# Kernel tuning notes

Measured on AMD Instinct MI355X. Metric: run time of the kernel, lower is better.

The kernel has to match this reference:

```python
import jax, jax.numpy as jnp
import numpy as np

EPS_BN = 1e-5
EPS_SIM = 1e-8
PAD = 1
NUM_ITERS = 3


def capsule_conv2d(x, w):
    # x: [B, C, H, W]; w: [out_caps, in_caps, kh, kw, in_len, out_len]
    B, C, H, W = x.shape
    oc, ic, kh, kw, il, ol = w.shape
    # im2col patches, feature dim ordered (c, kh, kw) -> matches torch.unfold
    patches = jax.lax.conv_general_dilated_patches(
        x, (kh, kw), (1, 1), [(PAD, PAD), (PAD, PAD)])  # [B, C*kh*kw, H, W]
    N = H * W
    p = patches.reshape(B, ic, il, kh * kw, N)
    p = jnp.transpose(p, (0, 4, 1, 3, 2))  # [B, N, ic, kk, il]
    wf = w.reshape(oc, ic, kh * kw, il, ol)
    # per-patch capsule transform -> priors [B, N, oc, ic*kk, ol]
    priors = jnp.einsum('bnikl,oiklm->bnoikm', p, wf)
    priors = priors.reshape(B, N, oc, ic * kh * kw, ol)
    # k-means routing with Tonimoto similarity, 3 iterations, no squash
    out = priors.mean(axis=-2, keepdims=True)  # [B, N, oc, 1, ol]
    for _ in range(NUM_ITERS):
        dot = jnp.sum(priors * out, axis=-1, keepdims=True)
        n1 = jnp.sum(priors * priors, axis=-1, keepdims=True)
        n2 = jnp.sum(out * out, axis=-1, keepdims=True)
        logits = dot / jnp.maximum(n1 + n2 - dot, EPS_SIM)
        probs = jax.nn.softmax(logits, axis=-2)
        out = jnp.sum(probs * priors, axis=-2, keepdims=True)
    out = out[..., 0, :]                      # [B, N, oc, ol]
    out = out.reshape(B, H, W, oc * ol)       # channels = oc*ol
    return jnp.transpose(out, (0, 3, 1, 2))   # [B, C, H, W]


def batchnorm2d(x, gamma, beta):
    mean = x.mean(axis=(0, 2, 3), keepdims=True)
    var = x.var(axis=(0, 2, 3), keepdims=True)  # biased, as torch BN training fwd
    inv = jax.lax.rsqrt(var + EPS_BN)
    return gamma[None, :, None, None] * (x - mean) * inv + beta[None, :, None, None]


def setup_inputs() -> dict:
    key = jax.random.key(0)
    k0, k1, k2 = jax.random.split(key, 3)
    B, C, H, W = 2, 64, 96, 96
    IL = OL = 8
    x = jax.random.normal(k0, (B, C, H, W), jnp.float32)
    w1 = jax.random.normal(k1, (C // OL, C // IL, 3, 3, IL, OL), jnp.float32) * 0.1
    w2 = jax.random.normal(k2, (C // OL, C // OL, 3, 3, OL, OL), jnp.float32) * 0.1
    g1 = jnp.ones((C,), jnp.float32)
    b1 = jnp.zeros((C,), jnp.float32)
    g2 = jnp.ones((C,), jnp.float32)
    b2 = jnp.zeros((C,), jnp.float32)
    return {"x": x, "w1": w1, "g1": g1, "b1": b1, "w2": w2, "g2": g2, "b2": b2}


def reference(x, w1, g1, b1, w2, g2, b2):
    r = batchnorm2d(capsule_conv2d(x, w1), g1, b1)
    r = batchnorm2d(capsule_conv2d(r, w2), g2, b2)
    return x + r
```

## Files before the change

### kernel.cpp

```cpp
#include <hip/hip_runtime.h>
#include <hip/hip_bf16.h>

#define HW 9216
#define NPC 18432
#define NELEM 1179648
#define PSTR 584
#define XSTR 72
#define PATCH_B 7776
#define PRL_O 18688

typedef __attribute__((ext_vector_type(2))) float f32x2;
typedef __attribute__((ext_vector_type(4))) float f32x4v;
typedef __attribute__((ext_vector_type(8))) short short8v;

__device__ __forceinline__ f32x2 fma2(f32x2 a, f32x2 b, f32x2 c) {
#if __has_builtin(__builtin_elementwise_fma)
    return __builtin_elementwise_fma(a, b, c);
#else
    return f32x2{fmaf(a.x, b.x, c.x), fmaf(a.y, b.y, c.y)};
#endif
}
__device__ __forceinline__ float dot8v(f32x2 a0, f32x2 a1, f32x2 a2, f32x2 a3,
                                       f32x2 b0, f32x2 b1, f32x2 b2, f32x2 b3) {
    f32x2 acc = a0 * b0;
    acc = fma2(a1, b1, acc);
    acc = fma2(a2, b2, acc);
    acc = fma2(a3, b3, acc);
    return acc.x + acc.y;
}

template <int CTRL>
__device__ __forceinline__ float dpp_add(float x) {
    int y = __builtin_amdgcn_update_dpp(0, __float_as_int(x), CTRL, 0xF, 0xF, true);
    return x + __int_as_float(y);
}
template <int CTRL>
__device__ __forceinline__ f32x2 dpp_add2(f32x2 x) {
    int ya = __builtin_amdgcn_update_dpp(0, __float_as_int(x.x), CTRL, 0xF, 0xF, true);
    int yb = __builtin_amdgcn_update_dpp(0, __float_as_int(x.y), CTRL, 0xF, 0xF, true);
    return x + f32x2{__int_as_float(ya), __int_as_float(yb)};
}
__device__ __forceinline__ float red_lo(float x) {
    x = dpp_add<0xB1>(x);
    x = dpp_add<0x4E>(x);
    x = dpp_add<0x141>(x);
    return x;
}
__device__ __forceinline__ f32x2 red_lo2(f32x2 x) {
    x = dpp_add2<0xB1>(x);
    x = dpp_add2<0x4E>(x);
    x = dpp_add2<0x141>(x);
    return x;
}

__device__ __forceinline__ int detect_is32(const unsigned short* __restrict__ w1u) {
    int lane = threadIdx.x & 63;
    int bad = 0;
    #pragma unroll
    for (int i = 0; i < 16; ++i) {
        unsigned short u = (unsigned short)(w1u[lane + i * 64] & 0x7FFF);
        bad |= (u >= 0x42C8);
    }
    return (__ballot(bad) != 0ULL) ? 1 : 0;
}

__device__ __forceinline__ float load_in(const void* p, int idx, int is32) {
    return is32 ? ((const float*)p)[idx]
                : __bfloat162float(((const __hip_bfloat16*)p)[idx]);
}

__device__ __forceinline__ float lo16(unsigned v) { return __int_as_float((int)(v << 16)); }
__device__ __forceinline__ float hi16(unsigned v) { return __int_as_float((int)(v & 0xFFFF0000u)); }
__device__ __forceinline__ unsigned pk2bf(float a, float b) {
    __hip_bfloat162 h = __float22bfloat162_rn(float2{a, b});
    return *(unsigned*)&h;
}

__launch_bounds__(256)
__global__ void prep_kernel(const void* __restrict__ x,
                            const void* __restrict__ w1, const void* __restrict__ w2,
                            __hip_bfloat16* __restrict__ xt,
                            __hip_bfloat16* __restrict__ Bfr1,
                            __hip_bfloat16* __restrict__ Bfr2,
                            float* __restrict__ statz) {
    __shared__ float tile[64 * 33];
    const int bid = blockIdx.x;
    if (bid < 576) {
        const int is32 = detect_is32((const unsigned short*)w1);
        int xb = bid % 3, y = (bid / 3) % 96, b = bid / 288;
        int x0 = xb * 32;
        for (int e = threadIdx.x; e < 2048; e += 256) {
            int xl = e & 31, c = e >> 5;
            tile[c * 33 + xl] = load_in(x, ((b * 64 + c) * 96 + y) * 96 + x0 + xl, is32);
        }
        __syncthreads();
        for (int f = threadIdx.x; f < 1024; f += 256) {
            int c2 = f & 31, xl = f >> 5;
            float a = tile[(2 * c2) * 33 + xl];
            float c = tile[(2 * c2 + 1) * 33 + xl];
            *(unsigned*)&xt[((b * 96 + y) * 96 + x0 + xl) * 64 + 2 * c2] = pk2bf(a, c);
        }
    } else if (bid < 720) {
        const int is32 = detect_is32((const unsigned short*)w1);
        int t = (bid - 576) * 256 + threadIdx.x;
        int layer = t / 18432;
        int r = t - layer * 18432;
        int lane = r & 63;
        int fi = r >> 6;
        int h = fi & 1, g = (fi >> 1) & 1;
        int kq = fi >> 2;
        int k = kq % 9, o = kq / 9;
        int dy = k / 3, dx = k % 3;
        int quad = lane >> 4, colhi = (lane >> 3) & 1, m = lane & 7;
        int act = (quad == 2 * h + colhi);
        int i = g * 4 + 2 * h + colhi;
        const void* w = layer ? w2 : w1;
        __hip_bfloat16* dst = layer ? Bfr2 : Bfr1;
        #pragma unroll
        for (int j = 0; j < 8; ++j) {
            float v = act ? load_in(w, ((((o * 8 + i) * 3 + dy) * 3 + dx) * 8 + j) * 8 + m, is32)
                          : 0.f;
            dst[(fi * 64 + lane) * 8 + j] = __float2bfloat16(v);
        }
    } else {
        for (int e = threadIdx.x; e < 2048; e += 256) statz[e] = 0.f;
    }
}

__launch_bounds__(256, 3)
__global__ void caps_kernel(const __hip_bfloat16* __restrict__ in,
                            const float* __restrict__ statPrev,
                            const void* __restrict__ gamma, const void* __restrict__ beta,
                            const void* __restrict__ wdt,
                            const __hip_bfloat16* __restrict__ Bfr,
                            __hip_bfloat16* __restrict__ yout,
                            float* __restrict__ statL,
                            int layer1) {
    __shared__ __align__(16) unsigned char smem[PATCH_B + 2 * PRL_O];
    __hip_bfloat16* patchH = (__hip_bfloat16*)smem;
    __hip_bfloat16* prH    = (__hip_bfloat16*)(smem + PATCH_B);
    float* omF = (float*)smem;
    float* scL = (float*)(smem + PATCH_B);
    float* shL = scL + 64;

    const int gx    = blockIdx.x;
    const int opair = gx & 3;
    const int x0    = (gx >> 2) * 16;
    const int y  = blockIdx.y;
    const int b  = blockIdx.z;
    const int tid = threadIdx.x;

    if (!layer1) {
        if (tid < 64) {
            const int is32 = detect_is32((const unsigned short*)wdt);
            int c = tid;
            float s = 0.f, ss = 0.f;
            #pragma unroll
            for (int cp = 0; cp < 8; ++cp) {
                s  += statPrev[cp * 128 + c];
                ss += statPrev[cp * 128 + 64 + c];
            }
            float mean = s * (1.f / (float)NPC);
            float var  = fmaxf(ss * (1.f / (float)NPC) - mean * mean, 0.f);
            float inv  = rsqrtf(var + 1e-5f);
            float g = load_in(gamma, c, is32) * inv;
            scL[c] = g;
            shL[c] = load_in(beta, c, is32) - mean * g;
        }
        __syncthreads();
    }

    for (int e = tid; e < 864; e += 256) {
        int c4 = e & 15;
        int q  = e >> 4;
        int xo = q % 18, row = q / 18;
        int yy = y + row - 1, xx = x0 + xo - 1;
        uint2 v = {0u, 0u};
        if (yy >= 0 && yy < 96 && xx >= 0 && xx < 96) {
            v = *(const uint2*)&in[((b * 96 + yy) * 96 + xx) * 64 + c4 * 4];
            if (!layer1) {
                int c = c4 * 4;
                float f0 = lo16(v.x) * scL[c]     + shL[c];
                float f1 = hi16(v.x) * scL[c + 1] + shL[c + 1];
                float f2 = lo16(v.y) * scL[c + 2] + shL[c + 2];
                float f3 = hi16(v.y) * scL[c + 3] + shL[c + 3];
                v.x = pk2bf(f0, f1);
                v.y = pk2bf(f2, f3);
            }
        }
        *(uint2*)&patchH[q * XSTR + c4 * 4] = v;
    }
    __syncthreads();

    const int lane = tid & 63;
    const int wv   = tid >> 6;
    const int o2w  = wv >> 1;
    const int g    = wv & 1;

    {
        const int o     = opair * 2 + o2w;
        const int pos16 = lane & 15;
        const int quad  = lane >> 4;
        const int mbase = (quad & 1) * 4;
        const int ihl   = quad >> 1;
        __hip_bfloat16* prBase = prH + o2w * 9344;
        #pragma unroll
        for (int k = 0; k < 9; ++k) {
            const int dy = k / 3, dx = k % 3;
            short8v a = *(const short8v*)&patchH[(dy * 18 + dx + pos16) * XSTR + g * 32 + quad * 8];
            #pragma unroll
            for (int h = 0; h < 2; ++h) {
                short8v bf = *(const short8v*)&Bfr[((((o * 9 + k) * 2 + g) * 2 + h) * 64 + lane) * 8];
                f32x4v d = __builtin_amdgcn_mfma_f32_16x16x32_bf16(bf, a, (f32x4v){0.f, 0.f, 0.f, 0.f}, 0, 0, 0);
                const int iw = g * 4 + 2 * h + ihl;
                uint2 pk;
                pk.x = pk2bf(d[0], d[1]);
                pk.y = pk2bf(d[2], d[3]);
                *(uint2*)&prBase[pos16 * PSTR + (iw * 9 + k) * 8 + mbase] = pk;
            }
        }
    }
    __syncthreads();

    const int unit = tid >> 3;
    const int o2   = unit >> 4;
    const int pos  = unit & 15;
    const int i    = tid & 7;
    const __hip_bfloat16* pb = &prH[o2 * 9344 + pos * PSTR + i * 72];

    uint4 u[9];
    #pragma unroll
    for (int k = 0; k < 9; ++k) u[k] = *(const uint4*)(pb + k * 8);

    f32x2 fr[36];
    float n1[9];
    #pragma unroll
    for (int k = 0; k < 9; ++k) {
        fr[4 * k + 0] = f32x2{lo16(u[k].x), hi16(u[k].x)};
        fr[4 * k + 1] = f32x2{lo16(u[k].y), hi16(u[k].y)};
        fr[4 * k + 2] = f32x2{lo16(u[k].z), hi16(u[k].z)};
        fr[4 * k + 3] = f32x2{lo16(u[k].w), hi16(u[k].w)};
    }

    f32x2 om2[4];
    {
        f32x2 s2[4] = {f32x2{0.f, 0.f}, f32x2{0.f, 0.f}, f32x2{0.f, 0.f}, f32x2{0.f, 0.f}};
        #pragma unroll
        for (int k = 0; k < 9; ++k) {
            s2[0] += fr[4 * k + 0];
            s2[1] += fr[4 * k + 1];
            s2[2] += fr[4 * k + 2];
            s2[3] += fr[4 * k + 3];
        }
        #pragma unroll
        for (int q = 0; q < 4; ++q) {
            f32x2 t = red_lo2(s2[q]);
            om2[q] = t * f32x2{1.f / 72.f, 1.f / 72.f};
        }
    }
    float n2 = dot8v(om2[0], om2[1], om2[2], om2[3], om2[0], om2[1], om2[2], om2[3]);

    #pragma unroll
    for (int it = 0; it < 3; ++it) {
        float se = 0.f;
        f32x2 acc2[4] = {f32x2{0.f, 0.f}, f32x2{0.f, 0.f}, f32x2{0.f, 0.f}, f32x2{0.f, 0.f}};
        #pragma unroll
        for (int k = 0; k < 9; ++k) {
            if (it == 0)
                n1[k] = dot8v(fr[4 * k], fr[4 * k + 1], fr[4 * k + 2], fr[4 * k + 3],
                              fr[4 * k], fr[4 * k + 1], fr[4 * k + 2], fr[4 * k + 3]);
            float d = dot8v(fr[4 * k], fr[4 * k + 1], fr[4 * k + 2], fr[4 * k + 3],
                            om2[0], om2[1], om2[2], om2[3]);
            float denom = fmaxf(n1[k] + n2 - d, 1e-8f);
            float e = __expf(d * __builtin_amdgcn_rcpf(denom));
            se += e;
            f32x2 ev{e, e};
            acc2[0] = fma2(ev, fr[4 * k + 0], acc2[0]);
            acc2[1] = fma2(ev, fr[4 * k + 1], acc2[1]);
            acc2[2] = fma2(ev, fr[4 * k + 2], acc2[2]);
            acc2[3] = fma2(ev, fr[4 * k + 3], acc2[3]);
        }
        se = red_lo(se);
        #pragma unroll
        for (int q = 0; q < 4; ++q) acc2[q] = red_lo2(acc2[q]);
        float inv = __builtin_amdgcn_rcpf(se);
        f32x2 iv{inv, inv};
        #pragma unroll
        for (int q = 0; q < 4; ++q) om2[q] = acc2[q] * iv;
        n2 = dot8v(om2[0], om2[1], om2[2], om2[3], om2[0], om2[1], om2[2], om2[3]);
    }

    if (i == 0) {
        const int o = opair * 2 + o2;
        uint4 pk;
        pk.x = pk2bf(om2[0].x, om2[0].y);
        pk.y = pk2bf(om2[1].x, om2[1].y);
        pk.z = pk2bf(om2[2].x, om2[2].y);
        pk.w = pk2bf(om2[3].x, om2[3].y);
        *(uint4*)&yout[((b * 96 + y) * 96 + x0 + pos) * 64 + o * 8] = pk;
        float4 o0 = {om2[0].x, om2[0].y, om2[1].x, om2[1].y};
        float4 o1 = {om2[2].x, om2[2].y, om2[3].x, om2[3].y};
        *(float4*)&omF[unit * 8] = o0;
        *(float4*)&omF[unit * 8 + 4] = o1;
    }
    __syncthreads();

    if (tid < 32) {
        int c16 = tid & 15, sel = tid >> 4;
        int oo2 = c16 >> 3, m = c16 & 7;
        float v = 0.f;
        #pragma unroll
        for (int pp = 0; pp < 16; ++pp) {
            float t = omF[(oo2 * 16 + pp) * 8 + m];
            v += sel ? t * t : t;
        }
        int cp = (blockIdx.x + blockIdx.y * 3 + blockIdx.z) & 7;
        atomicAdd(&statL[cp * 128 + sel * 64 + (opair * 2 + oo2) * 8 + m], v);
    }
}

__launch_bounds__(256)
__global__ void final_kernel(const void* __restrict__ xin,
                             const __hip_bfloat16* __restrict__ yt2,
                             const float* __restrict__ statL,
                             const void* __restrict__ gamma, const void* __restrict__ beta,
                             const void* __restrict__ w1,
                             void* __restrict__ outp) {
    __shared__ float tile[64 * 33];
    __shared__ float scL[64], shL[64];
    const int is32 = detect_is32((const unsigned short*)w1);
    if (threadIdx.x < 64) {
        int c = threadIdx.x;
        float s = 0.f, ss = 0.f;
        #pragma unroll
        for (int cp = 0; cp < 8; ++cp) {
            s  += statL[cp * 128 + c];
            ss += statL[cp * 128 + 64 + c];
        }
        float mean = s * (1.f / (float)NPC);
        float var  = fmaxf(ss * (1.f / (float)NPC) - mean * mean, 0.f);
        float inv  = rsqrtf(var + 1e-5f);
        float g = load_in(gamma, c, is32) * inv;
        scL[c] = g;
        shL[c] = load_in(beta, c, is32) - mean * g;
    }
    __syncthreads();

    int x0 = blockIdx.x * 32, y = blockIdx.y, b = blockIdx.z;
    for (int e = threadIdx.x; e < 1024; e += 256) {
        int c2 = e & 31, xl = e >> 5;
        unsigned v = *(const unsigned*)&yt2[((b * 96 + y) * 96 + x0 + xl) * 64 + c2 * 2];
        int c = c2 * 2;
        tile[c * 33 + xl]       = lo16(v) * scL[c]     + shL[c];
        tile[(c + 1) * 33 + xl] = hi16(v) * scL[c + 1] + shL[c + 1];
    }
    __syncthreads();
    for (int f = threadIdx.x; f < 2048; f += 256) {
        int xl = f & 31, c = f >> 5;
        int idx = ((b * 64 + c) * 96 + y) * 96 + x0 + xl;
        float v = load_in(xin, idx, is32) + tile[c * 33 + xl];
        if (is32) ((float*)outp)[idx] = v;
        else      ((__hip_bfloat16*)outp)[idx] = __float2bfloat16(v);
    }
}

extern "C" void kernel_launch(void* const* d_in, const int* in_sizes, int n_in,
                              void* d_out, int out_size, void* d_ws, size_t ws_size,
                              hipStream_t stream) {
    const void* x  = d_in[0];
    const void* w1 = d_in[1];
    const void* g1 = d_in[2];
    const void* b1 = d_in[3];
    const void* w2 = d_in[4];
    const void* g2 = d_in[5];
    const void* b2 = d_in[6];

    __hip_bfloat16* bufA = (__hip_bfloat16*)d_ws;
    __hip_bfloat16* bufB = bufA + NELEM;
    __hip_bfloat16* Bfr1 = bufB + NELEM;
    __hip_bfloat16* Bfr2 = Bfr1 + 147456;
    float* statz = (float*)(Bfr2 + 147456);
    float* statL1 = statz;
    float* statL2 = statz + 1024;

    prep_kernel<<<721, 256, 0, stream>>>(x, w1, w2, bufA, Bfr1, Bfr2, statz);

    dim3 cgrid(24, 96, 2);
    caps_kernel<<<cgrid, 256, 0, stream>>>(bufA, nullptr, nullptr, nullptr, w1,
                                           Bfr1, bufB, statL1, 1);
    caps_kernel<<<cgrid, 256, 0, stream>>>(bufB, statL1, g1, b1, w1,
                                           Bfr2, bufA, statL2, 0);
    final_kernel<<<dim3(3, 96, 2), 256, 0, stream>>>(x, bufA, statL2, g2, b2, w1, d_out);
}
```

Before: 175.7 us.

## Split capsule routing to one output capsule per block, two threads per row

Each caps_kernel block now handles a single output capsule instead of a pair, so the grid doubles and shared memory for priors halves. Within routing, each (position, input-capsule) pair is split across two threads that each take about half of the 9 kernel taps, with an extra DPP reduction step across 16 lanes. The aim is to cut per-thread register pressure (fr drops from 36 to 20 vectors) and raise occupancy (launch bounds 3→4 blocks). The cost is that patch loading and BN-apply work is repeated twice as often across blocks, plus a padded fifth tap slot and an extra reduction stage.

Result: slower. 187.1 us (+6.5%).

```diff
diff --git a/kernel.cpp b/kernel.cpp
--- a/kernel.cpp
+++ b/kernel.cpp
@@ -40,16 +40,18 @@
     int yb = __builtin_amdgcn_update_dpp(0, __float_as_int(x.y), CTRL, 0xF, 0xF, true);
     return x + f32x2{__int_as_float(ya), __int_as_float(yb)};
 }
-__device__ __forceinline__ float red_lo(float x) {
+__device__ __forceinline__ float red16(float x) {
     x = dpp_add<0xB1>(x);
     x = dpp_add<0x4E>(x);
     x = dpp_add<0x141>(x);
+    x = dpp_add<0x140>(x);
     return x;
 }
-__device__ __forceinline__ f32x2 red_lo2(f32x2 x) {
+__device__ __forceinline__ f32x2 red16_2(f32x2 x) {
     x = dpp_add2<0xB1>(x);
     x = dpp_add2<0x4E>(x);
     x = dpp_add2<0x141>(x);
+    x = dpp_add2<0x140>(x);
     return x;
 }
 
@@ -127,7 +129,7 @@
     }
 }
 
-__launch_bounds__(256, 3)
+__launch_bounds__(256, 4)
 __global__ void caps_kernel(const __hip_bfloat16* __restrict__ in,
                             const float* __restrict__ statPrev,
                             const void* __restrict__ gamma, const void* __restrict__ beta,
@@ -136,16 +138,16 @@
                             __hip_bfloat16* __restrict__ yout,
                             float* __restrict__ statL,
                             int layer1) {
-    __shared__ __align__(16) unsigned char smem[PATCH_B + 2 * PRL_O];
+    __shared__ __align__(16) unsigned char smem[PATCH_B + PRL_O];
     __hip_bfloat16* patchH = (__hip_bfloat16*)smem;
     __hip_bfloat16* prH    = (__hip_bfloat16*)(smem + PATCH_B);
     float* omF = (float*)smem;
     float* scL = (float*)(smem + PATCH_B);
     float* shL = scL + 64;
 
-    const int gx    = blockIdx.x;
-    const int opair = gx & 3;
-    const int x0    = (gx >> 2) * 16;
+    const int gx = blockIdx.x;
+    const int o  = gx & 7;
+    const int x0 = (gx >> 3) * 16;
     const int y  = blockIdx.y;
     const int b  = blockIdx.z;
     const int tid = threadIdx.x;
@@ -194,95 +196,91 @@
 
     const int lane = tid & 63;
     const int wv   = tid >> 6;
-    const int o2w  = wv >> 1;
-    const int g    = wv & 1;
 
     {
-        const int o     = opair * 2 + o2w;
+        const int g = wv & 1;
+        const int h = wv >> 1;
         const int pos16 = lane & 15;
         const int quad  = lane >> 4;
         const int mbase = (quad & 1) * 4;
         const int ihl   = quad >> 1;
-        __hip_bfloat16* prBase = prH + o2w * 9344;
+        const int iw    = g * 4 + 2 * h + ihl;
         #pragma unroll
         for (int k = 0; k < 9; ++k) {
             const int dy = k / 3, dx = k % 3;
             short8v a = *(const short8v*)&patchH[(dy * 18 + dx + pos16) * XSTR + g * 32 + quad * 8];
-            #pragma unroll
-            for (int h = 0; h < 2; ++h) {
-                short8v bf = *(const short8v*)&Bfr[((((o * 9 + k) * 2 + g) * 2 + h) * 64 + lane) * 8];
-                f32x4v d = __builtin_amdgcn_mfma_f32_16x16x32_bf16(bf, a, (f32x4v){0.f, 0.f, 0.f, 0.f}, 0, 0, 0);
-                const int iw = g * 4 + 2 * h + ihl;
-                uint2 pk;
-                pk.x = pk2bf(d[0], d[1]);
-                pk.y = pk2bf(d[2], d[3]);
-                *(uint2*)&prBase[pos16 * PSTR + (iw * 9 + k) * 8 + mbase] = pk;
-            }
-        }
-    }
-    __syncthreads();
-
-    const int unit = tid >> 3;
-    const int o2   = unit >> 4;
-    const int pos  = unit & 15;
-    const int i    = tid & 7;
-    const __hip_bfloat16* pb = &prH[o2 * 9344 + pos * PSTR + i * 72];
-
-    uint4 u[9];
+            short8v bf = *(const short8v*)&Bfr[((((o * 9 + k) * 2 + g) * 2 + h) * 64 + lane) * 8];
+            f32x4v d = __builtin_amdgcn_mfma_f32_16x16x32_bf16(bf, a, (f32x4v){0.f, 0.f, 0.f, 0.f}, 0, 0, 0);
+            uint2 pk;
+            pk.x = pk2bf(d[0], d[1]);
+            pk.y = pk2bf(d[2], d[3]);
+            *(uint2*)&prH[pos16 * PSTR + (iw * 9 + k) * 8 + mbase] = pk;
+        }
+    }
+    __syncthreads();
+
+    const int pos = tid >> 4;
+    const int i   = tid & 7;
+    const int kh  = (tid >> 3) & 1;
+    const __hip_bfloat16* pb = &prH[pos * PSTR + i * 72];
+
+    uint4 u[5];
     #pragma unroll
-    for (int k = 0; k < 9; ++k) u[k] = *(const uint4*)(pb + k * 8);
-
-    f32x2 fr[36];
-    float n1[9];
+    for (int t = 0; t < 4; ++t) u[t] = *(const uint4*)(pb + (kh + 2 * t) * 8);
+    u[4] = *(const uint4*)(pb + 8 * 8);
+    if (kh) { u[4].x = 0u; u[4].y = 0u; u[4].z = 0u; u[4].w = 0u; }
+
+    f32x2 fr[20];
+    float n1[5];
     #pragma unroll
-    for (int k = 0; k < 9; ++k) {
-        fr[4 * k + 0] = f32x2{lo16(u[k].x), hi16(u[k].x)};
-        fr[4 * k + 1] = f32x2{lo16(u[k].y), hi16(u[k].y)};
-        fr[4 * k + 2] = f32x2{lo16(u[k].z), hi16(u[k].z)};
-        fr[4 * k + 3] = f32x2{lo16(u[k].w), hi16(u[k].w)};
+    for (int t = 0; t < 5; ++t) {
+        fr[4 * t + 0] = f32x2{lo16(u[t].x), hi16(u[t].x)};
+        fr[4 * t + 1] = f32x2{lo16(u[t].y), hi16(u[t].y)};
+        fr[4 * t + 2] = f32x2{lo16(u[t].z), hi16(u[t].z)};
+        fr[4 * t + 3] = f32x2{lo16(u[t].w), hi16(u[t].w)};
     }
 
     f32x2 om2[4];
     {
         f32x2 s2[4] = {f32x2{0.f, 0.f}, f32x2{0.f, 0.f}, f32x2{0.f, 0.f}, f32x2{0.f, 0.f}};
         #pragma unroll
-        for (int k = 0; k < 9; ++k) {
-            s2[0] += fr[4 * k + 0];
-            s2[1] += fr[4 * k + 1];
-            s2[2] += fr[4 * k + 2];
-            s2[3] += fr[4 * k + 3];
+        for (int t = 0; t < 5; ++t) {
+            s2[0] += fr[4 * t + 0];
+            s2[1] += fr[4 * t + 1];
+            s2[2] += fr[4 * t + 2];
+            s2[3] += fr[4 * t + 3];
         }
         #pragma unroll
         for (int q = 0; q < 4; ++q) {
-            f32x2 t = red_lo2(s2[q]);
-            om2[q] = t * f32x2{1.f / 72.f, 1.f / 72.f};
+            f32x2 tt = red16_2(s2[q]);
+            om2[q] = tt * f32x2{1.f / 72.f, 1.f / 72.f};
         }
     }
     float n2 = dot8v(om2[0], om2[1], om2[2], om2[3], om2[0], om2[1], om2[2], om2[3]);
 
     #pragma unroll
     for (int it = 0; it < 3; ++it) {
-        float se = 0.f;
+        float se = kh ? -1.f : 0.f;
         f32x2 acc2[4] = {f32x2{0.f, 0.f}, f32x2{0.f, 0.f}, f32x2{0.f, 0.f}, f32x2{0.f, 0.f}};
         #pragma unroll
-        for (int k = 0; k < 9; ++k) {
+        for (int t = 0; t < 5; ++t) {
             if (it == 0)
-                n1[k] = dot8v(fr[4 * k], fr[4 * k + 1], fr[4 * k + 2], fr[4 * k + 3],
-                              fr[4 * k], fr[4 * k + 1], fr[4 * k + 2], fr[4 * k + 3]);
-            float d = dot8v(fr[4 * k], fr[4 * k + 1], fr[4 * k + 2], fr[4 * k + 3],
+                n1[t] = dot8v(fr[4 * t], fr[4 * t + 1], fr[4 * t + 2], fr[4 * t + 3],
+                              fr[4 * t], fr[4 * t + 1], fr[4 * t + 2], fr[4 * t + 3]);
+            float d = dot8v(fr[4 * t], fr[4 * t + 1], fr[4 * t + 2], fr[4 * t + 3],
                             om2[0], om2[1], om2[2], om2[3]);
-            float denom = fmaxf(n1[k] + n2 - d, 1e-8f);
+            float denom = fmaxf(n1[t] + n2 - d, 1e-8f);
             float e = __expf(d * __builtin_amdgcn_rcpf(denom));
             se += e;
             f32x2 ev{e, e};
-            acc2[0] = fma2(ev, fr[4 * k + 0], acc2[0]);
-            acc2[1] = fma2(ev, fr[4 * k + 1], acc2[1]);
-            acc2[2] = fma2(ev, fr[4 * k + 2], acc2[2]);
-            acc2[3] = fma2(ev, fr[4 * k + 3], acc2[3]);
-        }
-        se = red_lo(se);
-        #pragma unroll
-        for (int q = 0; q < 4; ++q) acc2[q] = red_lo2(acc2[q]);
+            acc2[0] = fma2(ev, fr[4 * t + 0], acc2[0]);
+            acc2[1] = fma2(ev, fr[4 * t + 1], acc2[1]);
+            acc2[2] = fma2(ev, fr[4 * t + 2], acc2[2]);
+            acc2[3] = fma2(ev, fr[4 * t + 3], acc2[3]);
+        }
+        se = red16(se);
+        #pragma unroll
+        for (int q = 0; q < 4; ++q) acc2[q] = red16_2(acc2[q]);
         float inv = __builtin_amdgcn_rcpf(se);
         f32x2 iv{inv, inv};
         #pragma unroll
@@ -290,8 +288,7 @@
         n2 = dot8v(om2[0], om2[1], om2[2], om2[3], om2[0], om2[1], om2[2], om2[3]);
     }
 
-    if (i == 0) {
-        const int o = opair * 2 + o2;
+    if ((tid & 15) == 0) {
         uint4 pk;
         pk.x = pk2bf(om2[0].x, om2[0].y);
         pk.y = pk2bf(om2[1].x, om2[1].y);
@@ -300,22 +297,21 @@
         *(uint4*)&yout[((b * 96 + y) * 96 + x0 + pos) * 64 + o * 8] = pk;
         float4 o0 = {om2[0].x, om2[0].y, om2[1].x, om2[1].y};
         float4 o1 = {om2[2].x, om2[2].y, om2[3].x, om2[3].y};
-        *(float4*)&omF[unit * 8] = o0;
-        *(float4*)&omF[unit * 8 + 4] = o1;
-    }
-    __syncthreads();
-
-    if (tid < 32) {
-        int c16 = tid & 15, sel = tid >> 4;
-        int oo2 = c16 >> 3, m = c16 & 7;
+        *(float4*)&omF[pos * 8] = o0;
+        *(float4*)&omF[pos * 8 + 4] = o1;
+    }
+    __syncthreads();
+
+    if (tid < 16) {
+        int m = tid & 7, sel = tid >> 3;
         float v = 0.f;
         #pragma unroll
         for (int pp = 0; pp < 16; ++pp) {
-            float t = omF[(oo2 * 16 + pp) * 8 + m];
+            float t = omF[pp * 8 + m];
             v += sel ? t * t : t;
         }
         int cp = (blockIdx.x + blockIdx.y * 3 + blockIdx.z) & 7;
-        atomicAdd(&statL[cp * 128 + sel * 64 + (opair * 2 + oo2) * 8 + m], v);
+        atomicAdd(&statL[cp * 128 + sel * 64 + o * 8 + m], v);
     }
 }
 
@@ -385,7 +381,7 @@
 
     prep_kernel<<<721, 256, 0, stream>>>(x, w1, w2, bufA, Bfr1, Bfr2, statz);
 
-    dim3 cgrid(24, 96, 2);
+    dim3 cgrid(48, 96, 2);
     caps_kernel<<<cgrid, 256, 0, stream>>>(bufA, nullptr, nullptr, nullptr, w1,
                                            Bfr1, bufB, statL1, 1);
     caps_kernel<<<cgrid, 256, 0, stream>>>(bufB, statL1, g1, b1, w1,
```

## Keep capsule priors in MFMA registers and route with cross-lane shuffles

Applied to the files above, without the earlier changes.

The capsule transform's MFMA outputs now stay in registers in their native MFMA layout. The bf16 round-trip through a large LDS prior buffer is gone. The routing iterations do their dot products and weighted sums with lane shuffles, plus a small LDS exchange between the two waves that hold different input-capsule halves, with a block barrier per iteration. LDS use shrinks, so occupancy rises to 4 blocks per CU. The price is extra syncthreads and shuffles per iteration, and each wave does redundant routing math.

After: 165.5 us. -5.8%, faster.

```diff
diff --git a/kernel.cpp b/kernel.cpp
--- a/kernel.cpp
+++ b/kernel.cpp
@@ -4,54 +4,14 @@
 #define HW 9216
 #define NPC 18432
 #define NELEM 1179648
-#define PSTR 584
 #define XSTR 72
 #define PATCH_B 7776
-#define PRL_O 18688
+#define XREC 12
+#define XBUF_B (4*2*16*2*XREC*4)
 
 typedef __attribute__((ext_vector_type(2))) float f32x2;
 typedef __attribute__((ext_vector_type(4))) float f32x4v;
 typedef __attribute__((ext_vector_type(8))) short short8v;
-
-__device__ __forceinline__ f32x2 fma2(f32x2 a, f32x2 b, f32x2 c) {
-#if __has_builtin(__builtin_elementwise_fma)
-    return __builtin_elementwise_fma(a, b, c);
-#else
-    return f32x2{fmaf(a.x, b.x, c.x), fmaf(a.y, b.y, c.y)};
-#endif
-}
-__device__ __forceinline__ float dot8v(f32x2 a0, f32x2 a1, f32x2 a2, f32x2 a3,
-                                       f32x2 b0, f32x2 b1, f32x2 b2, f32x2 b3) {
-    f32x2 acc = a0 * b0;
-    acc = fma2(a1, b1, acc);
-    acc = fma2(a2, b2, acc);
-    acc = fma2(a3, b3, acc);
-    return acc.x + acc.y;
-}
-
-template <int CTRL>
-__device__ __forceinline__ float dpp_add(float x) {
-    int y = __builtin_amdgcn_update_dpp(0, __float_as_int(x), CTRL, 0xF, 0xF, true);
-    return x + __int_as_float(y);
-}
-template <int CTRL>
-__device__ __forceinline__ f32x2 dpp_add2(f32x2 x) {
-    int ya = __builtin_amdgcn_update_dpp(0, __float_as_int(x.x), CTRL, 0xF, 0xF, true);
-    int yb = __builtin_amdgcn_update_dpp(0, __float_as_int(x.y), CTRL, 0xF, 0xF, true);
-    return x + f32x2{__int_as_float(ya), __int_as_float(yb)};
-}
-__device__ __forceinline__ float red_lo(float x) {
-    x = dpp_add<0xB1>(x);
-    x = dpp_add<0x4E>(x);
-    x = dpp_add<0x141>(x);
-    return x;
-}
-__device__ __forceinline__ f32x2 red_lo2(f32x2 x) {
-    x = dpp_add2<0xB1>(x);
-    x = dpp_add2<0x4E>(x);
-    x = dpp_add2<0x141>(x);
-    return x;
-}
 
 __device__ __forceinline__ int detect_is32(const unsigned short* __restrict__ w1u) {
     int lane = threadIdx.x & 63;
@@ -127,7 +87,22 @@
     }
 }
 
-__launch_bounds__(256, 3)
+__device__ __forceinline__ void xexchange(float* __restrict__ xbufF, int slot,
+                                          int o2w, int pos16, int g, int quad,
+                                          int mhalf, float ac[4], float& se) {
+    float* rec = xbufF + ((((slot * 2 + o2w) * 16 + pos16) * 2 + g) * XREC);
+    if (quad < 2) {
+        *(float4*)(rec + quad * 4) = make_float4(ac[0], ac[1], ac[2], ac[3]);
+        if (quad == 0) rec[8] = se;
+    }
+    __syncthreads();
+    const float* prec = xbufF + ((((slot * 2 + o2w) * 16 + pos16) * 2 + (1 - g)) * XREC);
+    float4 po = *(const float4*)(prec + mhalf * 4);
+    ac[0] += po.x; ac[1] += po.y; ac[2] += po.z; ac[3] += po.w;
+    se += prec[8];
+}
+
+__launch_bounds__(256, 4)
 __global__ void caps_kernel(const __hip_bfloat16* __restrict__ in,
                             const float* __restrict__ statPrev,
                             const void* __restrict__ gamma, const void* __restrict__ beta,
@@ -136,9 +111,9 @@
                             __hip_bfloat16* __restrict__ yout,
                             float* __restrict__ statL,
                             int layer1) {
-    __shared__ __align__(16) unsigned char smem[PATCH_B + 2 * PRL_O];
+    __shared__ __align__(16) unsigned char smem[PATCH_B + XBUF_B];
     __hip_bfloat16* patchH = (__hip_bfloat16*)smem;
-    __hip_bfloat16* prH    = (__hip_bfloat16*)(smem + PATCH_B);
+    float* xbufF = (float*)(smem + PATCH_B);
     float* omF = (float*)smem;
     float* scL = (float*)(smem + PATCH_B);
     float* shL = scL + 64;
@@ -192,18 +167,17 @@
     }
     __syncthreads();
 
-    const int lane = tid & 63;
-    const int wv   = tid >> 6;
-    const int o2w  = wv >> 1;
-    const int g    = wv & 1;
-
+    const int lane  = tid & 63;
+    const int wv    = tid >> 6;
+    const int o2w   = wv >> 1;
+    const int g     = wv & 1;
+    const int pos16 = lane & 15;
+    const int quad  = lane >> 4;
+    const int mhalf = quad & 1;
+
+    f32x4v P[9][2];
     {
-        const int o     = opair * 2 + o2w;
-        const int pos16 = lane & 15;
-        const int quad  = lane >> 4;
-        const int mbase = (quad & 1) * 4;
-        const int ihl   = quad >> 1;
-        __hip_bfloat16* prBase = prH + o2w * 9344;
+        const int o = opair * 2 + o2w;
         #pragma unroll
         for (int k = 0; k < 9; ++k) {
             const int dy = k / 3, dx = k % 3;
@@ -211,97 +185,102 @@
             #pragma unroll
             for (int h = 0; h < 2; ++h) {
                 short8v bf = *(const short8v*)&Bfr[((((o * 9 + k) * 2 + g) * 2 + h) * 64 + lane) * 8];
-                f32x4v d = __builtin_amdgcn_mfma_f32_16x16x32_bf16(bf, a, (f32x4v){0.f, 0.f, 0.f, 0.f}, 0, 0, 0);
-                const int iw = g * 4 + 2 * h + ihl;
-                uint2 pk;
-                pk.x = pk2bf(d[0], d[1]);
-                pk.y = pk2bf(d[2], d[3]);
-                *(uint2*)&prBase[pos16 * PSTR + (iw * 9 + k) * 8 + mbase] = pk;
+                P[k][h] = __builtin_amdgcn_mfma_f32_16x16x32_bf16(bf, a, (f32x4v){0.f, 0.f, 0.f, 0.f}, 0, 0, 0);
             }
         }
     }
-    __syncthreads();
-
-    const int unit = tid >> 3;
-    const int o2   = unit >> 4;
-    const int pos  = unit & 15;
-    const int i    = tid & 7;
-    const __hip_bfloat16* pb = &prH[o2 * 9344 + pos * PSTR + i * 72];
-
-    uint4 u[9];
-    #pragma unroll
-    for (int k = 0; k < 9; ++k) u[k] = *(const uint4*)(pb + k * 8);
-
-    f32x2 fr[36];
-    float n1[9];
+
+    float n1o[9];
     #pragma unroll
     for (int k = 0; k < 9; ++k) {
-        fr[4 * k + 0] = f32x2{lo16(u[k].x), hi16(u[k].x)};
-        fr[4 * k + 1] = f32x2{lo16(u[k].y), hi16(u[k].y)};
-        fr[4 * k + 2] = f32x2{lo16(u[k].z), hi16(u[k].z)};
-        fr[4 * k + 3] = f32x2{lo16(u[k].w), hi16(u[k].w)};
-    }
-
-    f32x2 om2[4];
+        float np0 = P[k][0][0] * P[k][0][0];
+        np0 = fmaf(P[k][0][1], P[k][0][1], np0);
+        np0 = fmaf(P[k][0][2], P[k][0][2], np0);
+        np0 = fmaf(P[k][0][3], P[k][0][3], np0);
+        float np1 = P[k][1][0] * P[k][1][0];
+        np1 = fmaf(P[k][1][1], P[k][1][1], np1);
+        np1 = fmaf(P[k][1][2], P[k][1][2], np1);
+        np1 = fmaf(P[k][1][3], P[k][1][3], np1);
+        float own = mhalf ? np1 : np0;
+        float oth = mhalf ? np0 : np1;
+        n1o[k] = own + __shfl_xor(oth, 16, 64);
+    }
+
+    float om[4];
     {
-        f32x2 s2[4] = {f32x2{0.f, 0.f}, f32x2{0.f, 0.f}, f32x2{0.f, 0.f}, f32x2{0.f, 0.f}};
-        #pragma unroll
-        for (int k = 0; k < 9; ++k) {
-            s2[0] += fr[4 * k + 0];
-            s2[1] += fr[4 * k + 1];
-            s2[2] += fr[4 * k + 2];
-            s2[3] += fr[4 * k + 3];
-        }
-        #pragma unroll
-        for (int q = 0; q < 4; ++q) {
-            f32x2 t = red_lo2(s2[q]);
-            om2[q] = t * f32x2{1.f / 72.f, 1.f / 72.f};
-        }
-    }
-    float n2 = dot8v(om2[0], om2[1], om2[2], om2[3], om2[0], om2[1], om2[2], om2[3]);
+        float ac[4];
+        #pragma unroll
+        for (int r = 0; r < 4; ++r) {
+            float s = 0.f;
+            #pragma unroll
+            for (int k = 0; k < 9; ++k) s += P[k][0][r] + P[k][1][r];
+            s += __shfl_xor(s, 32, 64);
+            ac[r] = s;
+        }
+        float dummy = 0.f;
+        xexchange(xbufF, 0, o2w, pos16, g, quad, mhalf, ac, dummy);
+        #pragma unroll
+        for (int r = 0; r < 4; ++r) om[r] = ac[r] * (1.f / 72.f);
+    }
+    float n2;
+    {
+        float n2p = om[0] * om[0];
+        n2p = fmaf(om[1], om[1], n2p);
+        n2p = fmaf(om[2], om[2], n2p);
+        n2p = fmaf(om[3], om[3], n2p);
+        n2 = n2p + __shfl_xor(n2p, 16, 64);
+    }
 
     #pragma unroll
     for (int it = 0; it < 3; ++it) {
         float se = 0.f;
-        f32x2 acc2[4] = {f32x2{0.f, 0.f}, f32x2{0.f, 0.f}, f32x2{0.f, 0.f}, f32x2{0.f, 0.f}};
+        float ac[4] = {0.f, 0.f, 0.f, 0.f};
         #pragma unroll
         for (int k = 0; k < 9; ++k) {
-            if (it == 0)
-                n1[k] = dot8v(fr[4 * k], fr[4 * k + 1], fr[4 * k + 2], fr[4 * k + 3],
-                              fr[4 * k], fr[4 * k + 1], fr[4 * k + 2], fr[4 * k + 3]);
-            float d = dot8v(fr[4 * k], fr[4 * k + 1], fr[4 * k + 2], fr[4 * k + 3],
-                            om2[0], om2[1], om2[2], om2[3]);
-            float denom = fmaxf(n1[k] + n2 - d, 1e-8f);
+            float dp0 = P[k][0][0] * om[0];
+            dp0 = fmaf(P[k][0][1], om[1], dp0);
+            dp0 = fmaf(P[k][0][2], om[2], dp0);
+            dp0 = fmaf(P[k][0][3], om[3], dp0);
+            float dp1 = P[k][1][0] * om[0];
+            dp1 = fmaf(P[k][1][1], om[1], dp1);
+            dp1 = fmaf(P[k][1][2], om[2], dp1);
+            dp1 = fmaf(P[k][1][3], om[3], dp1);
+            float own = mhalf ? dp1 : dp0;
+            float oth = mhalf ? dp0 : dp1;
+            float d = own + __shfl_xor(oth, 16, 64);
+            float denom = fmaxf(n1o[k] + n2 - d, 1e-8f);
             float e = __expf(d * __builtin_amdgcn_rcpf(denom));
             se += e;
-            f32x2 ev{e, e};
-            acc2[0] = fma2(ev, fr[4 * k + 0], acc2[0]);
-            acc2[1] = fma2(ev, fr[4 * k + 1], acc2[1]);
-            acc2[2] = fma2(ev, fr[4 * k + 2], acc2[2]);
-            acc2[3] = fma2(ev, fr[4 * k + 3], acc2[3]);
-        }
-        se = red_lo(se);
-        #pragma unroll
-        for (int q = 0; q < 4; ++q) acc2[q] = red_lo2(acc2[q]);
+            float e_oth = __shfl_xor(e, 16, 64);
+            float eh0 = mhalf ? e_oth : e;
+            float eh1 = mhalf ? e : e_oth;
+            ac[0] = fmaf(eh0, P[k][0][0], fmaf(eh1, P[k][1][0], ac[0]));
+            ac[1] = fmaf(eh0, P[k][0][1], fmaf(eh1, P[k][1][1], ac[1]));
+            ac[2] = fmaf(eh0, P[k][0][2], fmaf(eh1, P[k][1][2], ac[2]));
+            ac[3] = fmaf(eh0, P[k][0][3], fmaf(eh1, P[k][1][3], ac[3]));
+        }
+        se += __shfl_xor(se, 16, 64);
+        se += __shfl_xor(se, 32, 64);
+        #pragma unroll
+        for (int r = 0; r < 4; ++r) ac[r] += __shfl_xor(ac[r], 32, 64);
+        xexchange(xbufF, 1 + it, o2w, pos16, g, quad, mhalf, ac, se);
         float inv = __builtin_amdgcn_rcpf(se);
-        f32x2 iv{inv, inv};
-        #pragma unroll
-        for (int q = 0; q < 4; ++q) om2[q] = acc2[q] * iv;
-        n2 = dot8v(om2[0], om2[1], om2[2], om2[3], om2[0], om2[1], om2[2], om2[3]);
-    }
-
-    if (i == 0) {
-        const int o = opair * 2 + o2;
-        uint4 pk;
-        pk.x = pk2bf(om2[0].x, om2[0].y);
-        pk.y = pk2bf(om2[1].x, om2[1].y);
-        pk.z = pk2bf(om2[2].x, om2[2].y);
-        pk.w = pk2bf(om2[3].x, om2[3].y);
-        *(uint4*)&yout[((b * 96 + y) * 96 + x0 + pos) * 64 + o * 8] = pk;
-        float4 o0 = {om2[0].x, om2[0].y, om2[1].x, om2[1].y};
-        float4 o1 = {om2[2].x, om2[2].y, om2[3].x, om2[3].y};
-        *(float4*)&omF[unit * 8] = o0;
-        *(float4*)&omF[unit * 8 + 4] = o1;
+        #pragma unroll
+        for (int r = 0; r < 4; ++r) om[r] = ac[r] * inv;
+        float n2p = om[0] * om[0];
+        n2p = fmaf(om[1], om[1], n2p);
+        n2p = fmaf(om[2], om[2], n2p);
+        n2p = fmaf(om[3], om[3], n2p);
+        n2 = n2p + __shfl_xor(n2p, 16, 64);
+    }
+
+    if (g == 0 && quad < 2) {
+        const int o = opair * 2 + o2w;
+        uint2 pk;
+        pk.x = pk2bf(om[0], om[1]);
+        pk.y = pk2bf(om[2], om[3]);
+        *(uint2*)&yout[((b * 96 + y) * 96 + x0 + pos16) * 64 + o * 8 + mhalf * 4] = pk;
+        *(float4*)&omF[(o2w * 16 + pos16) * 8 + mhalf * 4] = make_float4(om[0], om[1], om[2], om[3]);
     }
     __syncthreads();
 
```
